# Kernel tuning notes

Hardware: AMD Instinct MI355X
Metric: run time of the kernel (lower is better)

The kernel has to match this reference:

```python
import jax, jax.numpy as jnp
import numpy as np


def _up2(x):
    return jnp.repeat(jnp.repeat(x, 2, axis=2), 2, axis=3)


def setup_inputs() -> dict:
    key = jax.random.key(0)
    ks = jax.random.split(key, 6)
    Vps, C, H, W = 32, 128, 64, 64
    return {
        "x1": jax.random.normal(ks[0], (Vps, C, H, W), dtype=jnp.float32),
        "x2": jax.random.normal(ks[1], (Vps, C, H // 2, W // 2), dtype=jnp.float32),
        "x3": jax.random.normal(ks[2], (Vps, C, H // 4, W // 4), dtype=jnp.float32),
        "x4": jax.random.normal(ks[3], (Vps, C, H // 4, W // 4), dtype=jnp.float32),
        "conv_w": jax.random.normal(ks[4], (128, 512), dtype=jnp.float32) * 0.02,
        "conv_b": jnp.zeros((128,), dtype=jnp.float32),
        "gamma": jnp.zeros((1,), dtype=jnp.float32),
        "weight": jnp.ones((128,), dtype=jnp.float32),
        "lin_w": jax.random.normal(ks[5], (1, 128), dtype=jnp.float32) * 0.1,
    }


def reference(x1, x2, x3, x4, conv_w, conv_b, gamma, weight, lin_w):
    # upsample lower pyramid levels to x1 resolution and concat on channels
    x_sm = jnp.concatenate([x1, _up2(x2), _up2(_up2(x3)), _up2(_up2(x4))], axis=1)
    # 1x1 conv: [Vps,512,H,W] x [128,512] -> [Vps,128,H,W]
    x_sm = jnp.einsum('vchw,oc->vohw', x_sm, conv_w) + conv_b[None, :, None, None]
    Vps, C, H, W = x_sm.shape

    # --- batch (viewport) attention ---
    gap = jnp.mean(x_sm, axis=(2, 3))                     # [Vps, C]
    v_q = gap @ lin_w.T                                    # [Vps, 1]
    att = v_q @ v_q.T                                      # [Vps, Vps]
    att_new = jnp.broadcast_to(jnp.max(att, axis=-1, keepdims=True), att.shape)
    vps_mat = jax.nn.softmax(att_new, axis=-1)             # rows constant -> uniform
    v_v = x_sm.reshape(Vps, C * H * W)
    vps_att = (vps_mat @ v_v).reshape(Vps, C, H, W)
    x_sm = vps_att * gamma + x_sm

    # --- channel attention ---
    c_q = jnp.mean(x_sm, axis=(2, 3))                      # [Vps, C]
    att_C = c_q.T @ c_q                                    # [C, C]
    C_mat = jax.nn.softmax(att_C, axis=-1) * weight        # broadcast over last dim
    c_v = x_sm.reshape(C, Vps * H * W)                     # faithful raw reshape as in torch
    C_att = (C_mat @ c_v).reshape(Vps, C, H, W)
    out = C_att + x_sm
    return out.reshape(Vps, C, H * W)
```

## Files before the change

### kernel.cpp

```cpp
#include <hip/hip_runtime.h>

#define V 32
#define CH 128
#define SP 4096

typedef __attribute__((ext_vector_type(8))) short bf16x8;
typedef __attribute__((ext_vector_type(4))) float f32x4;

__device__ __forceinline__ unsigned short bf16rne(float x) {
    union { float f; unsigned u; } v; v.f = x;
    unsigned r = v.u + 0x7fff + ((v.u >> 16) & 1);
    return (unsigned short)(r >> 16);
}

__device__ __forceinline__ int xswz(int s) { return (s & 7) ^ ((s >> 2) & 7); }

__device__ __forceinline__ const float* xsm_row(const float* xsm, int j, int r) {
    return xsm + ((size_t)((j >> 2) * CH + (j & 3) * 32 + r)) * SP;
}

__global__ __launch_bounds__(256) void prep_w(const float* __restrict__ W,
                                              unsigned short* __restrict__ Wpad)
{
    int row = blockIdx.x;
    int j = threadIdx.x;
    if (j < 136) {
        int sigma = row >> 7, o = row & 127;
        float v = (j < 128) ? W[o * 512 + sigma * 128 + j] : 0.f;
        Wpad[row * 136 + j] = bf16rne(v);
    }
}

__global__ __launch_bounds__(256, 4) void conv_lo(
    const float* __restrict__ xa, const float* __restrict__ xb,
    const unsigned short* __restrict__ WA, const unsigned short* __restrict__ WB,
    int spatial, int nph, float* __restrict__ outbuf)
{
    __shared__ __align__(16) unsigned short Xl[64 * 128];
    const int v = blockIdx.y, sc = blockIdx.x, tid = threadIdx.x;
    const int lane = tid & 63, w = tid >> 6;
    const int l15 = lane & 15, quad = lane >> 4;
    const int o0 = (w >> 1) * 64, s0 = (w & 1) * 32;
    const int sq = tid & 15, cp0 = tid >> 4;

    f32x4 acc[4][2];
#pragma unroll
    for (int it = 0; it < 4; ++it)
#pragma unroll
        for (int st = 0; st < 2; ++st) acc[it][st] = (f32x4){0.f, 0.f, 0.f, 0.f};

#pragma unroll 1
    for (int ph = 0; ph < nph; ++ph) {
        if (ph) __syncthreads();
        const float* xp = ph ? xb : xa;
        const unsigned short* wp = ph ? WB : WA;
        const float* xbase = xp + (size_t)v * CH * spatial + sc * 64;
#pragma unroll
        for (int rep = 0; rep < 4; ++rep) {
            int c = (cp0 + rep * 16) * 2;
            const float* r0 = xbase + (size_t)c * spatial + sq * 4;
            float4 va = *(const float4*)r0;
            float4 vb = *(const float4*)(r0 + spatial);
            float a4[4] = {va.x, va.y, va.z, va.w};
            float b4[4] = {vb.x, vb.y, vb.z, vb.w};
#pragma unroll
            for (int i = 0; i < 4; ++i) {
                int s = sq * 4 + i;
                ushort2 pk; pk.x = bf16rne(a4[i]); pk.y = bf16rne(b4[i]);
                *(ushort2*)&Xl[s * 128 + (((c >> 3) ^ xswz(s)) * 8) + (c & 7)] = pk;
            }
        }
        __syncthreads();
#pragma unroll
        for (int ks = 0; ks < 4; ++ks) {
            int kb = ks * 4 + quad;
            bf16x8 af[4], bfr[2];
#pragma unroll
            for (int it = 0; it < 4; ++it)
                af[it] = *(const bf16x8*)&wp[(o0 + it * 16 + l15) * 136 + ks * 32 + quad * 8];
#pragma unroll
            for (int st = 0; st < 2; ++st) {
                int s = s0 + st * 16 + l15;
                bfr[st] = *(const bf16x8*)&Xl[s * 128 + ((kb ^ xswz(s)) * 8)];
            }
#pragma unroll
            for (int it = 0; it < 4; ++it)
#pragma unroll
                for (int st = 0; st < 2; ++st)
                    acc[it][st] = __builtin_amdgcn_mfma_f32_16x16x32_bf16(
                        bfr[st], af[it], acc[it][st], 0, 0, 0);
        }
    }
#pragma unroll
    for (int it = 0; it < 4; ++it) {
        int o = o0 + it * 16 + l15;
        float* orow = outbuf + ((size_t)(v * CH + o)) * spatial + sc * 64;
#pragma unroll
        for (int st = 0; st < 2; ++st) {
            int sb = s0 + st * 16 + quad * 4;
            *(f32x4*)(orow + sb) = acc[it][st];
        }
    }
}

__global__ __launch_bounds__(256, 4) void conv_full(
    const float* __restrict__ x1, const unsigned short* __restrict__ W0,
    const float* __restrict__ bias, const float* __restrict__ conv2,
    const float* __restrict__ conv34, float* __restrict__ xsm,
    float* __restrict__ gap)
{
    __shared__ __align__(16) unsigned short Xl[64 * 128];
    __shared__ float gscr[4][64];
    const int v = blockIdx.y, sc = blockIdx.x, tid = threadIdx.x;
    const int lane = tid & 63, w = tid >> 6;
    const int l15 = lane & 15, quad = lane >> 4;
    const int o0 = (w >> 1) * 64, s0 = (w & 1) * 32;
    const int sq = tid & 15, cp0 = tid >> 4;

    f32x4 acc[4][2];
#pragma unroll
    for (int it = 0; it < 4; ++it)
#pragma unroll
        for (int st = 0; st < 2; ++st) acc[it][st] = (f32x4){0.f, 0.f, 0.f, 0.f};

    const float* xbase = x1 + (size_t)v * CH * SP + sc * 64;
#pragma unroll
    for (int rep = 0; rep < 4; ++rep) {
        int c = (cp0 + rep * 16) * 2;
        const float* r0 = xbase + (size_t)c * SP + sq * 4;
        float4 va = *(const float4*)r0;
        float4 vb = *(const float4*)(r0 + SP);
        float a4[4] = {va.x, va.y, va.z, va.w};
        float b4[4] = {vb.x, vb.y, vb.z, vb.w};
#pragma unroll
        for (int i = 0; i < 4; ++i) {
            int s = sq * 4 + i;
            ushort2 pk; pk.x = bf16rne(a4[i]); pk.y = bf16rne(b4[i]);
            *(ushort2*)&Xl[s * 128 + (((c >> 3) ^ xswz(s)) * 8) + (c & 7)] = pk;
        }
    }
    __syncthreads();
#pragma unroll
    for (int ks = 0; ks < 4; ++ks) {
        int kb = ks * 4 + quad;
        bf16x8 af[4], bfr[2];
#pragma unroll
        for (int it = 0; it < 4; ++it)
            af[it] = *(const bf16x8*)&W0[(o0 + it * 16 + l15) * 136 + ks * 32 + quad * 8];
#pragma unroll
        for (int st = 0; st < 2; ++st) {
            int s = s0 + st * 16 + l15;
            bfr[st] = *(const bf16x8*)&Xl[s * 128 + ((kb ^ xswz(s)) * 8)];
        }
#pragma unroll
        for (int it = 0; it < 4; ++it)
#pragma unroll
            for (int st = 0; st < 2; ++st)
                acc[it][st] = __builtin_amdgcn_mfma_f32_16x16x32_bf16(
                    bfr[st], af[it], acc[it][st], 0, 0, 0);
    }

    const float* c2row = conv2 + (size_t)v * CH * 1024 + (sc >> 1) * 32;
    const float* c34row = conv34 + (size_t)v * CH * 256 + (sc >> 2) * 16;
    float gs[4];
#pragma unroll
    for (int it = 0; it < 4; ++it) {
        int o = o0 + it * 16 + l15;
        float b = bias[o];
        float* orow = xsm + ((size_t)(v * CH + o)) * SP + sc * 64;
        const float* c2p = c2row + (size_t)o * 1024;
        const float* c34p = c34row + (size_t)o * 256;
        float lsum = 0.f;
#pragma unroll
        for (int st = 0; st < 2; ++st) {
            int sb = s0 + st * 16 + quad * 4;
            float2 c2v = *(const float2*)(c2p + (sb >> 1));
            float c34v = c34p[sb >> 2];
            f32x4 a = acc[it][st];
            f32x4 ov;
            ov[0] = a[0] + b + c2v.x + c34v;
            ov[1] = a[1] + b + c2v.x + c34v;
            ov[2] = a[2] + b + c2v.y + c34v;
            ov[3] = a[3] + b + c2v.y + c34v;
            *(f32x4*)(orow + sb) = ov;
            lsum += ov[0] + ov[1] + ov[2] + ov[3];
        }
        gs[it] = lsum;
    }
#pragma unroll
    for (int m = 16; m < 64; m <<= 1)
#pragma unroll
        for (int k = 0; k < 4; ++k) gs[k] += __shfl_xor(gs[k], m, 64);
    if (quad == 0) {
#pragma unroll
        for (int it = 0; it < 4; ++it)
            gscr[w][it * 16 + l15] = gs[it];
    }
    __syncthreads();
    if (tid < 128) {
        int o = tid, b2 = (o >> 6) * 2;
        atomicAdd(&gap[v * CH + o], gscr[b2][o & 63] + gscr[b2 + 1][o & 63]);
    }
}

__global__ __launch_bounds__(128) void build_G(
    const float* __restrict__ gap, const float* __restrict__ gammap,
    const float* __restrict__ weight, unsigned short* __restrict__ GsPad)
{
    __shared__ float cq[32][128];
    __shared__ float red[128];
    const int i = blockIdx.x, j = threadIdx.x;
    const float g = gammap[0];

    float gb = 0.f;
    for (int v = 0; v < 32; ++v) gb += gap[v * CH + j];
    gb = gb * (1.f / 32.f) * (1.f / 4096.f) * g;
    for (int v = 0; v < 32; ++v) cq[v][j] = gap[v * CH + j] * (1.f / 4096.f) + gb;
    __syncthreads();

    float a = 0.f;
    for (int v = 0; v < 32; ++v) a += cq[v][i] * cq[v][j];

    red[j] = a; __syncthreads();
    float m = -1e30f;
    for (int t = 0; t < 128; ++t) m = fmaxf(m, red[t]);
    __syncthreads();
    float e = __expf(a - m);
    red[j] = e; __syncthreads();
    float ssum = 0.f;
    for (int t = 0; t < 128; ++t) ssum += red[t];
    float cm = e / ssum * weight[j] + ((i == j) ? 1.f : 0.f);
    __syncthreads();
    red[j] = cm; __syncthreads();
    float rs = 0.f;
    for (int t = (j & 3); t < 128; t += 4) rs += red[t];
    float gfull = cm + g * (1.f / 32.f) * rs;
    GsPad[i * 136 + j] = bf16rne(gfull - ((i == j) ? 1.f : 0.f));
}

__global__ __launch_bounds__(256, 4) void apply_G(
    float* __restrict__ xsm, const unsigned short* __restrict__ GsPad)
{
    __shared__ __align__(16) unsigned short Xl[64 * 128];
    const int r = blockIdx.y, sc = blockIdx.x, tid = threadIdx.x;
    const int lane = tid & 63, w = tid >> 6;
    const int l15 = lane & 15, quad = lane >> 4;
    const int i0 = (w >> 1) * 64, s0 = (w & 1) * 32;
    const int sq = tid & 15, cp0 = tid >> 4;

    f32x4 acc[4][2];
#pragma unroll
    for (int it = 0; it < 4; ++it)
#pragma unroll
        for (int st = 0; st < 2; ++st) acc[it][st] = (f32x4){0.f, 0.f, 0.f, 0.f};

#pragma unroll
    for (int rep = 0; rep < 4; ++rep) {
        int c = (cp0 + rep * 16) * 2;
        const float* r0 = xsm_row(xsm, c, r) + sc * 64 + sq * 4;
        const float* r1 = xsm_row(xsm, c + 1, r) + sc * 64 + sq * 4;
        float4 va = *(const float4*)r0;
        float4 vb = *(const float4*)r1;
        float a4[4] = {va.x, va.y, va.z, va.w};
        float b4[4] = {vb.x, vb.y, vb.z, vb.w};
#pragma unroll
        for (int i = 0; i < 4; ++i) {
            int s = sq * 4 + i;
            ushort2 pk; pk.x = bf16rne(a4[i]); pk.y = bf16rne(b4[i]);
            *(ushort2*)&Xl[s * 128 + (((c >> 3) ^ xswz(s)) * 8) + (c & 7)] = pk;
        }
    }
    __syncthreads();
#pragma unroll
    for (int ks = 0; ks < 4; ++ks) {
        int kb = ks * 4 + quad;
        bf16x8 af[4], bfr[2];
#pragma unroll
        for (int it = 0; it < 4; ++it)
            af[it] = *(const bf16x8*)&GsPad[(i0 + it * 16 + l15) * 136 + ks * 32 + quad * 8];
#pragma unroll
        for (int st = 0; st < 2; ++st) {
            int s = s0 + st * 16 + l15;
            bfr[st] = *(const bf16x8*)&Xl[s * 128 + ((kb ^ xswz(s)) * 8)];
        }
#pragma unroll
        for (int it = 0; it < 4; ++it)
#pragma unroll
            for (int st = 0; st < 2; ++st)
                acc[it][st] = __builtin_amdgcn_mfma_f32_16x16x32_bf16(
                    bfr[st], af[it], acc[it][st], 0, 0, 0);
    }
#pragma unroll
    for (int it = 0; it < 4; ++it) {
        int i = i0 + it * 16 + l15;
        float* rowp = (float*)xsm_row(xsm, i, r) + sc * 64;
#pragma unroll
        for (int st = 0; st < 2; ++st) {
            int sb = s0 + st * 16 + quad * 4;
            f32x4 res = *(const f32x4*)(rowp + sb);
            res += acc[it][st];
            *(f32x4*)(rowp + sb) = res;
        }
    }
}

extern "C" void kernel_launch(void* const* d_in, const int* in_sizes, int n_in,
                              void* d_out, int out_size, void* d_ws, size_t ws_size,
                              hipStream_t stream)
{
    const float* x1     = (const float*)d_in[0];
    const float* x2     = (const float*)d_in[1];
    const float* x3     = (const float*)d_in[2];
    const float* x4     = (const float*)d_in[3];
    const float* conv_w = (const float*)d_in[4];
    const float* conv_b = (const float*)d_in[5];
    const float* gamma  = (const float*)d_in[6];
    const float* weight = (const float*)d_in[7];

    float* out = (float*)d_out;
    float* ws  = (float*)d_ws;

    float* conv2  = ws;
    float* conv34 = ws + (size_t)4194304;
    float* gap    = ws + (size_t)5242880;
    unsigned short* Wpad  = (unsigned short*)(ws + (size_t)5246976);
    unsigned short* GsPad = (unsigned short*)(ws + (size_t)5281792);

    hipMemsetAsync(gap, 0, 4096 * sizeof(float), stream);

    prep_w<<<512, 256, 0, stream>>>(conv_w, Wpad);
    conv_lo<<<dim3(16, 32), 256, 0, stream>>>(x2, x2, Wpad + 1 * 128 * 136,
                                              Wpad + 1 * 128 * 136, 1024, 1, conv2);
    conv_lo<<<dim3(4, 32), 256, 0, stream>>>(x3, x4, Wpad + 2 * 128 * 136,
                                             Wpad + 3 * 128 * 136, 256, 2, conv34);
    conv_full<<<dim3(64, 32), 256, 0, stream>>>(x1, Wpad, conv_b, conv2, conv34, out, gap);
    build_G<<<128, 128, 0, stream>>>(gap, gamma, weight, GsPad);
    apply_G<<<dim3(64, 32), 256, 0, stream>>>(out, GsPad);
}
```

Baseline: 230.7 us.

## Make conv_full and apply_G persistent over four tiles with double-buffered LDS prefetch

Result: slower. 238.3 us (+3.3%).

```diff
diff --git a/kernel.cpp b/kernel.cpp
--- a/kernel.cpp
+++ b/kernel.cpp
@@ -31,7 +31,7 @@
     }
 }
 
-__global__ __launch_bounds__(256, 4) void conv_lo(
+__global__ __launch_bounds__(256, 3) void conv_lo(
     const float* __restrict__ xa, const float* __restrict__ xb,
     const unsigned short* __restrict__ WA, const unsigned short* __restrict__ WB,
     int spatial, int nph, float* __restrict__ outbuf)
@@ -54,6 +54,12 @@
         if (ph) __syncthreads();
         const float* xp = ph ? xb : xa;
         const unsigned short* wp = ph ? WB : WA;
+        bf16x8 af[4][4];
+#pragma unroll
+        for (int ks = 0; ks < 4; ++ks)
+#pragma unroll
+            for (int it = 0; it < 4; ++it)
+                af[ks][it] = *(const bf16x8*)&wp[(o0 + it * 16 + l15) * 136 + ks * 32 + quad * 8];
         const float* xbase = xp + (size_t)v * CH * spatial + sc * 64;
 #pragma unroll
         for (int rep = 0; rep < 4; ++rep) {
@@ -74,10 +80,7 @@
 #pragma unroll
         for (int ks = 0; ks < 4; ++ks) {
             int kb = ks * 4 + quad;
-            bf16x8 af[4], bfr[2];
-#pragma unroll
-            for (int it = 0; it < 4; ++it)
-                af[it] = *(const bf16x8*)&wp[(o0 + it * 16 + l15) * 136 + ks * 32 + quad * 8];
+            bf16x8 bfr[2];
 #pragma unroll
             for (int st = 0; st < 2; ++st) {
                 int s = s0 + st * 16 + l15;
@@ -88,7 +91,7 @@
 #pragma unroll
                 for (int st = 0; st < 2; ++st)
                     acc[it][st] = __builtin_amdgcn_mfma_f32_16x16x32_bf16(
-                        bfr[st], af[it], acc[it][st], 0, 0, 0);
+                        bfr[st], af[ks][it], acc[it][st], 0, 0, 0);
         }
     }
 #pragma unroll
@@ -103,103 +106,146 @@
     }
 }
 
-__global__ __launch_bounds__(256, 4) void conv_full(
+__global__ __launch_bounds__(256, 2) void conv_full(
     const float* __restrict__ x1, const unsigned short* __restrict__ W0,
     const float* __restrict__ bias, const float* __restrict__ conv2,
     const float* __restrict__ conv34, float* __restrict__ xsm,
     float* __restrict__ gap)
 {
-    __shared__ __align__(16) unsigned short Xl[64 * 128];
-    __shared__ float gscr[4][64];
-    const int v = blockIdx.y, sc = blockIdx.x, tid = threadIdx.x;
+    __shared__ __align__(16) unsigned short Xl[2][64 * 128];
+    const int vg = blockIdx.y, sc = blockIdx.x, tid = threadIdx.x;
     const int lane = tid & 63, w = tid >> 6;
     const int l15 = lane & 15, quad = lane >> 4;
     const int o0 = (w >> 1) * 64, s0 = (w & 1) * 32;
     const int sq = tid & 15, cp0 = tid >> 4;
 
-    f32x4 acc[4][2];
-#pragma unroll
-    for (int it = 0; it < 4; ++it)
-#pragma unroll
-        for (int st = 0; st < 2; ++st) acc[it][st] = (f32x4){0.f, 0.f, 0.f, 0.f};
-
-    const float* xbase = x1 + (size_t)v * CH * SP + sc * 64;
+    bf16x8 af[4][4];
+#pragma unroll
+    for (int ks = 0; ks < 4; ++ks)
+#pragma unroll
+        for (int it = 0; it < 4; ++it)
+            af[ks][it] = *(const bf16x8*)&W0[(o0 + it * 16 + l15) * 136 + ks * 32 + quad * 8];
+    float bv[4];
+#pragma unroll
+    for (int it = 0; it < 4; ++it) bv[it] = bias[o0 + it * 16 + l15];
+
+    float4 xva[4], xvb[4];
+    {
+        const float* xbase = x1 + (size_t)(vg * 4) * CH * SP + sc * 64;
+#pragma unroll
+        for (int rep = 0; rep < 4; ++rep) {
+            int c = (cp0 + rep * 16) * 2;
+            const float* r0 = xbase + (size_t)c * SP + sq * 4;
+            xva[rep] = *(const float4*)r0;
+            xvb[rep] = *(const float4*)(r0 + SP);
+        }
+    }
 #pragma unroll
     for (int rep = 0; rep < 4; ++rep) {
         int c = (cp0 + rep * 16) * 2;
-        const float* r0 = xbase + (size_t)c * SP + sq * 4;
-        float4 va = *(const float4*)r0;
-        float4 vb = *(const float4*)(r0 + SP);
-        float a4[4] = {va.x, va.y, va.z, va.w};
-        float b4[4] = {vb.x, vb.y, vb.z, vb.w};
+        float a4[4] = {xva[rep].x, xva[rep].y, xva[rep].z, xva[rep].w};
+        float b4[4] = {xvb[rep].x, xvb[rep].y, xvb[rep].z, xvb[rep].w};
 #pragma unroll
         for (int i = 0; i < 4; ++i) {
             int s = sq * 4 + i;
             ushort2 pk; pk.x = bf16rne(a4[i]); pk.y = bf16rne(b4[i]);
-            *(ushort2*)&Xl[s * 128 + (((c >> 3) ^ xswz(s)) * 8) + (c & 7)] = pk;
-        }
-    }
-    __syncthreads();
-#pragma unroll
-    for (int ks = 0; ks < 4; ++ks) {
-        int kb = ks * 4 + quad;
-        bf16x8 af[4], bfr[2];
+            *(ushort2*)&Xl[0][s * 128 + (((c >> 3) ^ xswz(s)) * 8) + (c & 7)] = pk;
+        }
+    }
+
+#pragma unroll 1
+    for (int t = 0; t < 4; ++t) {
+        const int v = vg * 4 + t;
+        __syncthreads();
+        if (t < 3) {
+            const float* xbase = x1 + (size_t)(v + 1) * CH * SP + sc * 64;
+#pragma unroll
+            for (int rep = 0; rep < 4; ++rep) {
+                int c = (cp0 + rep * 16) * 2;
+                const float* r0 = xbase + (size_t)c * SP + sq * 4;
+                xva[rep] = *(const float4*)r0;
+                xvb[rep] = *(const float4*)(r0 + SP);
+            }
+        }
+        const float* c2row = conv2 + (size_t)v * CH * 1024 + (sc >> 1) * 32;
+        const float* c34row = conv34 + (size_t)v * CH * 256 + (sc >> 2) * 16;
+        float2 c2v[4][2]; float c34v[4][2];
+#pragma unroll
+        for (int it = 0; it < 4; ++it) {
+            int o = o0 + it * 16 + l15;
+#pragma unroll
+            for (int st = 0; st < 2; ++st) {
+                int sb = s0 + st * 16 + quad * 4;
+                c2v[it][st] = *(const float2*)(c2row + (size_t)o * 1024 + (sb >> 1));
+                c34v[it][st] = c34row[(size_t)o * 256 + (sb >> 2)];
+            }
+        }
+        f32x4 acc[4][2];
 #pragma unroll
         for (int it = 0; it < 4; ++it)
-            af[it] = *(const bf16x8*)&W0[(o0 + it * 16 + l15) * 136 + ks * 32 + quad * 8];
-#pragma unroll
-        for (int st = 0; st < 2; ++st) {
-            int s = s0 + st * 16 + l15;
-            bfr[st] = *(const bf16x8*)&Xl[s * 128 + ((kb ^ xswz(s)) * 8)];
-        }
-#pragma unroll
-        for (int it = 0; it < 4; ++it)
-#pragma unroll
-            for (int st = 0; st < 2; ++st)
-                acc[it][st] = __builtin_amdgcn_mfma_f32_16x16x32_bf16(
-                    bfr[st], af[it], acc[it][st], 0, 0, 0);
-    }
-
-    const float* c2row = conv2 + (size_t)v * CH * 1024 + (sc >> 1) * 32;
-    const float* c34row = conv34 + (size_t)v * CH * 256 + (sc >> 2) * 16;
-    float gs[4];
-#pragma unroll
-    for (int it = 0; it < 4; ++it) {
-        int o = o0 + it * 16 + l15;
-        float b = bias[o];
-        float* orow = xsm + ((size_t)(v * CH + o)) * SP + sc * 64;
-        const float* c2p = c2row + (size_t)o * 1024;
-        const float* c34p = c34row + (size_t)o * 256;
-        float lsum = 0.f;
-#pragma unroll
-        for (int st = 0; st < 2; ++st) {
-            int sb = s0 + st * 16 + quad * 4;
-            float2 c2v = *(const float2*)(c2p + (sb >> 1));
-            float c34v = c34p[sb >> 2];
-            f32x4 a = acc[it][st];
-            f32x4 ov;
-            ov[0] = a[0] + b + c2v.x + c34v;
-            ov[1] = a[1] + b + c2v.x + c34v;
-            ov[2] = a[2] + b + c2v.y + c34v;
-            ov[3] = a[3] + b + c2v.y + c34v;
-            *(f32x4*)(orow + sb) = ov;
-            lsum += ov[0] + ov[1] + ov[2] + ov[3];
-        }
-        gs[it] = lsum;
-    }
-#pragma unroll
-    for (int m = 16; m < 64; m <<= 1)
-#pragma unroll
-        for (int k = 0; k < 4; ++k) gs[k] += __shfl_xor(gs[k], m, 64);
-    if (quad == 0) {
-#pragma unroll
-        for (int it = 0; it < 4; ++it)
-            gscr[w][it * 16 + l15] = gs[it];
-    }
-    __syncthreads();
-    if (tid < 128) {
-        int o = tid, b2 = (o >> 6) * 2;
-        atomicAdd(&gap[v * CH + o], gscr[b2][o & 63] + gscr[b2 + 1][o & 63]);
+#pragma unroll
+            for (int st = 0; st < 2; ++st) acc[it][st] = (f32x4){0.f, 0.f, 0.f, 0.f};
+        const unsigned short* Xcur = &Xl[t & 1][0];
+#pragma unroll
+        for (int ks = 0; ks < 4; ++ks) {
+            int kb = ks * 4 + quad;
+            bf16x8 bfr[2];
+#pragma unroll
+            for (int st = 0; st < 2; ++st) {
+                int s = s0 + st * 16 + l15;
+                bfr[st] = *(const bf16x8*)&Xcur[s * 128 + ((kb ^ xswz(s)) * 8)];
+            }
+#pragma unroll
+            for (int it = 0; it < 4; ++it)
+#pragma unroll
+                for (int st = 0; st < 2; ++st)
+                    acc[it][st] = __builtin_amdgcn_mfma_f32_16x16x32_bf16(
+                        bfr[st], af[ks][it], acc[it][st], 0, 0, 0);
+        }
+        float gs[4];
+#pragma unroll
+        for (int it = 0; it < 4; ++it) {
+            int o = o0 + it * 16 + l15;
+            float b = bv[it];
+            float* orow = xsm + ((size_t)(v * CH + o)) * SP + sc * 64;
+            float lsum = 0.f;
+#pragma unroll
+            for (int st = 0; st < 2; ++st) {
+                int sb = s0 + st * 16 + quad * 4;
+                f32x4 a = acc[it][st];
+                f32x4 ov;
+                ov[0] = a[0] + b + c2v[it][st].x + c34v[it][st];
+                ov[1] = a[1] + b + c2v[it][st].x + c34v[it][st];
+                ov[2] = a[2] + b + c2v[it][st].y + c34v[it][st];
+                ov[3] = a[3] + b + c2v[it][st].y + c34v[it][st];
+                *(f32x4*)(orow + sb) = ov;
+                lsum += ov[0] + ov[1] + ov[2] + ov[3];
+            }
+            gs[it] = lsum;
+        }
+#pragma unroll
+        for (int m = 16; m < 64; m <<= 1)
+#pragma unroll
+            for (int k = 0; k < 4; ++k) gs[k] += __shfl_xor(gs[k], m, 64);
+        if (quad == 0) {
+#pragma unroll
+            for (int it = 0; it < 4; ++it)
+                atomicAdd(&gap[v * CH + o0 + it * 16 + l15], gs[it]);
+        }
+        if (t < 3) {
+#pragma unroll
+            for (int rep = 0; rep < 4; ++rep) {
+                int c = (cp0 + rep * 16) * 2;
+                float a4[4] = {xva[rep].x, xva[rep].y, xva[rep].z, xva[rep].w};
+                float b4[4] = {xvb[rep].x, xvb[rep].y, xvb[rep].z, xvb[rep].w};
+#pragma unroll
+                for (int i = 0; i < 4; ++i) {
+                    int s = sq * 4 + i;
+                    ushort2 pk; pk.x = bf16rne(a4[i]); pk.y = bf16rne(b4[i]);
+                    *(ushort2*)&Xl[(t + 1) & 1][s * 128 + (((c >> 3) ^ xswz(s)) * 8) + (c & 7)] = pk;
+                }
+            }
+        }
     }
 }
 
@@ -238,68 +284,115 @@
     GsPad[i * 136 + j] = bf16rne(gfull - ((i == j) ? 1.f : 0.f));
 }
 
-__global__ __launch_bounds__(256, 4) void apply_G(
+__global__ __launch_bounds__(256, 2) void apply_G(
     float* __restrict__ xsm, const unsigned short* __restrict__ GsPad)
 {
-    __shared__ __align__(16) unsigned short Xl[64 * 128];
-    const int r = blockIdx.y, sc = blockIdx.x, tid = threadIdx.x;
+    __shared__ __align__(16) unsigned short Xl[2][64 * 128];
+    const int r = blockIdx.y, scg = blockIdx.x, tid = threadIdx.x;
     const int lane = tid & 63, w = tid >> 6;
     const int l15 = lane & 15, quad = lane >> 4;
     const int i0 = (w >> 1) * 64, s0 = (w & 1) * 32;
     const int sq = tid & 15, cp0 = tid >> 4;
 
-    f32x4 acc[4][2];
-#pragma unroll
-    for (int it = 0; it < 4; ++it)
-#pragma unroll
-        for (int st = 0; st < 2; ++st) acc[it][st] = (f32x4){0.f, 0.f, 0.f, 0.f};
-
+    bf16x8 af[4][4];
+#pragma unroll
+    for (int ks = 0; ks < 4; ++ks)
+#pragma unroll
+        for (int it = 0; it < 4; ++it)
+            af[ks][it] = *(const bf16x8*)&GsPad[(i0 + it * 16 + l15) * 136 + ks * 32 + quad * 8];
+
+    float4 xva[4], xvb[4];
+    {
+        const int sc = scg * 4;
+#pragma unroll
+        for (int rep = 0; rep < 4; ++rep) {
+            int c = (cp0 + rep * 16) * 2;
+            xva[rep] = *(const float4*)(xsm_row(xsm, c, r) + sc * 64 + sq * 4);
+            xvb[rep] = *(const float4*)(xsm_row(xsm, c + 1, r) + sc * 64 + sq * 4);
+        }
+    }
 #pragma unroll
     for (int rep = 0; rep < 4; ++rep) {
         int c = (cp0 + rep * 16) * 2;
-        const float* r0 = xsm_row(xsm, c, r) + sc * 64 + sq * 4;
-        const float* r1 = xsm_row(xsm, c + 1, r) + sc * 64 + sq * 4;
-        float4 va = *(const float4*)r0;
-        float4 vb = *(const float4*)r1;
-        float a4[4] = {va.x, va.y, va.z, va.w};
-        float b4[4] = {vb.x, vb.y, vb.z, vb.w};
+        float a4[4] = {xva[rep].x, xva[rep].y, xva[rep].z, xva[rep].w};
+        float b4[4] = {xvb[rep].x, xvb[rep].y, xvb[rep].z, xvb[rep].w};
 #pragma unroll
         for (int i = 0; i < 4; ++i) {
             int s = sq * 4 + i;
             ushort2 pk; pk.x = bf16rne(a4[i]); pk.y = bf16rne(b4[i]);
-            *(ushort2*)&Xl[s * 128 + (((c >> 3) ^ xswz(s)) * 8) + (c & 7)] = pk;
-        }
-    }
-    __syncthreads();
-#pragma unroll
-    for (int ks = 0; ks < 4; ++ks) {
-        int kb = ks * 4 + quad;
-        bf16x8 af[4], bfr[2];
+            *(ushort2*)&Xl[0][s * 128 + (((c >> 3) ^ xswz(s)) * 8) + (c & 7)] = pk;
+        }
+    }
+
+#pragma unroll 1
+    for (int t = 0; t < 4; ++t) {
+        const int sc = scg * 4 + t;
+        __syncthreads();
+        if (t < 3) {
+#pragma unroll
+            for (int rep = 0; rep < 4; ++rep) {
+                int c = (cp0 + rep * 16) * 2;
+                xva[rep] = *(const float4*)(xsm_row(xsm, c, r) + (sc + 1) * 64 + sq * 4);
+                xvb[rep] = *(const float4*)(xsm_row(xsm, c + 1, r) + (sc + 1) * 64 + sq * 4);
+            }
+        }
+        f32x4 resv[4][2];
+#pragma unroll
+        for (int it = 0; it < 4; ++it) {
+            int i = i0 + it * 16 + l15;
+            const float* rowp = xsm_row(xsm, i, r) + sc * 64;
+#pragma unroll
+            for (int st = 0; st < 2; ++st) {
+                int sb = s0 + st * 16 + quad * 4;
+                resv[it][st] = *(const f32x4*)(rowp + sb);
+            }
+        }
+        f32x4 acc[4][2];
 #pragma unroll
         for (int it = 0; it < 4; ++it)
-            af[it] = *(const bf16x8*)&GsPad[(i0 + it * 16 + l15) * 136 + ks * 32 + quad * 8];
-#pragma unroll
-        for (int st = 0; st < 2; ++st) {
-            int s = s0 + st * 16 + l15;
-            bfr[st] = *(const bf16x8*)&Xl[s * 128 + ((kb ^ xswz(s)) * 8)];
-        }
-#pragma unroll
-        for (int it = 0; it < 4; ++it)
-#pragma unroll
-            for (int st = 0; st < 2; ++st)
-                acc[it][st] = __builtin_amdgcn_mfma_f32_16x16x32_bf16(
-                    bfr[st], af[it], acc[it][st], 0, 0, 0);
-    }
-#pragma unroll
-    for (int it = 0; it < 4; ++it) {
-        int i = i0 + it * 16 + l15;
-        float* rowp = (float*)xsm_row(xsm, i, r) + sc * 64;
-#pragma unroll
-        for (int st = 0; st < 2; ++st) {
-            int sb = s0 + st * 16 + quad * 4;
-            f32x4 res = *(const f32x4*)(rowp + sb);
-            res += acc[it][st];
-            *(f32x4*)(rowp + sb) = res;
+#pragma unroll
+            for (int st = 0; st < 2; ++st) acc[it][st] = (f32x4){0.f, 0.f, 0.f, 0.f};
+        const unsigned short* Xcur = &Xl[t & 1][0];
+#pragma unroll
+        for (int ks = 0; ks < 4; ++ks) {
+            int kb = ks * 4 + quad;
+            bf16x8 bfr[2];
+#pragma unroll
+            for (int st = 0; st < 2; ++st) {
+                int s = s0 + st * 16 + l15;
+                bfr[st] = *(const bf16x8*)&Xcur[s * 128 + ((kb ^ xswz(s)) * 8)];
+            }
+#pragma unroll
+            for (int it = 0; it < 4; ++it)
+#pragma unroll
+                for (int st = 0; st < 2; ++st)
+                    acc[it][st] = __builtin_amdgcn_mfma_f32_16x16x32_bf16(
+                        bfr[st], af[ks][it], acc[it][st], 0, 0, 0);
+        }
+#pragma unroll
+        for (int it = 0; it < 4; ++it) {
+            int i = i0 + it * 16 + l15;
+            float* rowp = (float*)xsm_row(xsm, i, r) + sc * 64;
+#pragma unroll
+            for (int st = 0; st < 2; ++st) {
+                int sb = s0 + st * 16 + quad * 4;
+                f32x4 res = resv[it][st] + acc[it][st];
+                *(f32x4*)(rowp + sb) = res;
+            }
+        }
+        if (t < 3) {
+#pragma unroll
+            for (int rep = 0; rep < 4; ++rep) {
+                int c = (cp0 + rep * 16) * 2;
+                float a4[4] = {xva[rep].x, xva[rep].y, xva[rep].z, xva[rep].w};
+                float b4[4] = {xvb[rep].x, xvb[rep].y, xvb[rep].z, xvb[rep].w};
+#pragma unroll
+                for (int i = 0; i < 4; ++i) {
+                    int s = sq * 4 + i;
+                    ushort2 pk; pk.x = bf16rne(a4[i]); pk.y = bf16rne(b4[i]);
+                    *(ushort2*)&Xl[(t + 1) & 1][s * 128 + (((c >> 3) ^ xswz(s)) * 8) + (c & 7)] = pk;
+                }
+            }
         }
     }
 }
@@ -333,7 +426,7 @@
                                               Wpad + 1 * 128 * 136, 1024, 1, conv2);
     conv_lo<<<dim3(4, 32), 256, 0, stream>>>(x3, x4, Wpad + 2 * 128 * 136,
                                              Wpad + 3 * 128 * 136, 256, 2, conv34);
-    conv_full<<<dim3(64, 32), 256, 0, stream>>>(x1, Wpad, conv_b, conv2, conv34, out, gap);
+    conv_full<<<dim3(64, 8), 256, 0, stream>>>(x1, Wpad, conv_b, conv2, conv34, out, gap);
     build_G<<<128, 128, 0, stream>>>(gap, gamma, weight, GsPad);
-    apply_G<<<dim3(64, 32), 256, 0, stream>>>(out, GsPad);
-}
+    apply_G<<<dim3(16, 32), 256, 0, stream>>>(out, GsPad);
+}
```

## Load conv/apply operands directly from global into MFMA registers, drop LDS staging

Applied to the files above, without the earlier changes.

Result: slower. 244.6 us (+6.0%).

```diff
diff --git a/kernel.cpp b/kernel.cpp
--- a/kernel.cpp
+++ b/kernel.cpp
@@ -12,8 +12,6 @@
     unsigned r = v.u + 0x7fff + ((v.u >> 16) & 1);
     return (unsigned short)(r >> 16);
 }
-
-__device__ __forceinline__ int xswz(int s) { return (s & 7) ^ ((s >> 2) & 7); }
 
 __device__ __forceinline__ const float* xsm_row(const float* xsm, int j, int r) {
     return xsm + ((size_t)((j >> 2) * CH + (j & 3) * 32 + r)) * SP;
@@ -31,17 +29,15 @@
     }
 }
 
-__global__ __launch_bounds__(256, 4) void conv_lo(
+__global__ __launch_bounds__(256, 2) void conv_lo(
     const float* __restrict__ xa, const float* __restrict__ xb,
     const unsigned short* __restrict__ WA, const unsigned short* __restrict__ WB,
     int spatial, int nph, float* __restrict__ outbuf)
 {
-    __shared__ __align__(16) unsigned short Xl[64 * 128];
     const int v = blockIdx.y, sc = blockIdx.x, tid = threadIdx.x;
     const int lane = tid & 63, w = tid >> 6;
     const int l15 = lane & 15, quad = lane >> 4;
     const int o0 = (w >> 1) * 64, s0 = (w & 1) * 32;
-    const int sq = tid & 15, cp0 = tid >> 4;
 
     f32x4 acc[4][2];
 #pragma unroll
@@ -51,44 +47,35 @@
 
 #pragma unroll 1
     for (int ph = 0; ph < nph; ++ph) {
-        if (ph) __syncthreads();
         const float* xp = ph ? xb : xa;
         const unsigned short* wp = ph ? WB : WA;
-        const float* xbase = xp + (size_t)v * CH * spatial + sc * 64;
-#pragma unroll
-        for (int rep = 0; rep < 4; ++rep) {
-            int c = (cp0 + rep * 16) * 2;
-            const float* r0 = xbase + (size_t)c * spatial + sq * 4;
-            float4 va = *(const float4*)r0;
-            float4 vb = *(const float4*)(r0 + spatial);
-            float a4[4] = {va.x, va.y, va.z, va.w};
-            float b4[4] = {vb.x, vb.y, vb.z, vb.w};
-#pragma unroll
-            for (int i = 0; i < 4; ++i) {
-                int s = sq * 4 + i;
-                ushort2 pk; pk.x = bf16rne(a4[i]); pk.y = bf16rne(b4[i]);
-                *(ushort2*)&Xl[s * 128 + (((c >> 3) ^ xswz(s)) * 8) + (c & 7)] = pk;
+        bf16x8 af[4][4];
+#pragma unroll
+        for (int ks = 0; ks < 4; ++ks)
+#pragma unroll
+            for (int it = 0; it < 4; ++it)
+                af[ks][it] = *(const bf16x8*)&wp[(o0 + it * 16 + l15) * 136 + ks * 32 + quad * 8];
+        const float* xcol = xp + (size_t)v * CH * spatial + sc * 64;
+#pragma unroll
+        for (int st = 0; st < 2; ++st) {
+            const int sA = s0 + st * 16 + l15;
+            const float* xs = xcol + sA + (size_t)(quad * 8) * spatial;
+            float xr[4][8];
+#pragma unroll
+            for (int ks = 0; ks < 4; ++ks)
+#pragma unroll
+                for (int jj = 0; jj < 8; ++jj)
+                    xr[ks][jj] = xs[(size_t)(ks * 32 + jj) * spatial];
+#pragma unroll
+            for (int ks = 0; ks < 4; ++ks) {
+                bf16x8 bx;
+#pragma unroll
+                for (int jj = 0; jj < 8; ++jj) bx[jj] = (short)bf16rne(xr[ks][jj]);
+#pragma unroll
+                for (int it = 0; it < 4; ++it)
+                    acc[it][st] = __builtin_amdgcn_mfma_f32_16x16x32_bf16(
+                        bx, af[ks][it], acc[it][st], 0, 0, 0);
             }
-        }
-        __syncthreads();
-#pragma unroll
-        for (int ks = 0; ks < 4; ++ks) {
-            int kb = ks * 4 + quad;
-            bf16x8 af[4], bfr[2];
-#pragma unroll
-            for (int it = 0; it < 4; ++it)
-                af[it] = *(const bf16x8*)&wp[(o0 + it * 16 + l15) * 136 + ks * 32 + quad * 8];
-#pragma unroll
-            for (int st = 0; st < 2; ++st) {
-                int s = s0 + st * 16 + l15;
-                bfr[st] = *(const bf16x8*)&Xl[s * 128 + ((kb ^ xswz(s)) * 8)];
-            }
-#pragma unroll
-            for (int it = 0; it < 4; ++it)
-#pragma unroll
-                for (int st = 0; st < 2; ++st)
-                    acc[it][st] = __builtin_amdgcn_mfma_f32_16x16x32_bf16(
-                        bfr[st], af[it], acc[it][st], 0, 0, 0);
         }
     }
 #pragma unroll
@@ -103,19 +90,26 @@
     }
 }
 
-__global__ __launch_bounds__(256, 4) void conv_full(
+__global__ __launch_bounds__(256, 2) void conv_full(
     const float* __restrict__ x1, const unsigned short* __restrict__ W0,
     const float* __restrict__ bias, const float* __restrict__ conv2,
     const float* __restrict__ conv34, float* __restrict__ xsm,
     float* __restrict__ gap)
 {
-    __shared__ __align__(16) unsigned short Xl[64 * 128];
-    __shared__ float gscr[4][64];
     const int v = blockIdx.y, sc = blockIdx.x, tid = threadIdx.x;
     const int lane = tid & 63, w = tid >> 6;
     const int l15 = lane & 15, quad = lane >> 4;
     const int o0 = (w >> 1) * 64, s0 = (w & 1) * 32;
-    const int sq = tid & 15, cp0 = tid >> 4;
+
+    bf16x8 af[4][4];
+#pragma unroll
+    for (int ks = 0; ks < 4; ++ks)
+#pragma unroll
+        for (int it = 0; it < 4; ++it)
+            af[ks][it] = *(const bf16x8*)&W0[(o0 + it * 16 + l15) * 136 + ks * 32 + quad * 8];
+    float bv[4];
+#pragma unroll
+    for (int it = 0; it < 4; ++it) bv[it] = bias[o0 + it * 16 + l15];
 
     f32x4 acc[4][2];
 #pragma unroll
@@ -123,41 +117,27 @@
 #pragma unroll
         for (int st = 0; st < 2; ++st) acc[it][st] = (f32x4){0.f, 0.f, 0.f, 0.f};
 
-    const float* xbase = x1 + (size_t)v * CH * SP + sc * 64;
-#pragma unroll
-    for (int rep = 0; rep < 4; ++rep) {
-        int c = (cp0 + rep * 16) * 2;
-        const float* r0 = xbase + (size_t)c * SP + sq * 4;
-        float4 va = *(const float4*)r0;
-        float4 vb = *(const float4*)(r0 + SP);
-        float a4[4] = {va.x, va.y, va.z, va.w};
-        float b4[4] = {vb.x, vb.y, vb.z, vb.w};
-#pragma unroll
-        for (int i = 0; i < 4; ++i) {
-            int s = sq * 4 + i;
-            ushort2 pk; pk.x = bf16rne(a4[i]); pk.y = bf16rne(b4[i]);
-            *(ushort2*)&Xl[s * 128 + (((c >> 3) ^ xswz(s)) * 8) + (c & 7)] = pk;
-        }
-    }
-    __syncthreads();
-#pragma unroll
-    for (int ks = 0; ks < 4; ++ks) {
-        int kb = ks * 4 + quad;
-        bf16x8 af[4], bfr[2];
-#pragma unroll
-        for (int it = 0; it < 4; ++it)
-            af[it] = *(const bf16x8*)&W0[(o0 + it * 16 + l15) * 136 + ks * 32 + quad * 8];
-#pragma unroll
-        for (int st = 0; st < 2; ++st) {
-            int s = s0 + st * 16 + l15;
-            bfr[st] = *(const bf16x8*)&Xl[s * 128 + ((kb ^ xswz(s)) * 8)];
-        }
-#pragma unroll
-        for (int it = 0; it < 4; ++it)
-#pragma unroll
-            for (int st = 0; st < 2; ++st)
+    const float* xcol = x1 + (size_t)v * CH * SP + sc * 64;
+#pragma unroll
+    for (int st = 0; st < 2; ++st) {
+        const int sA = s0 + st * 16 + l15;
+        const float* xs = xcol + sA + (size_t)(quad * 8) * SP;
+        float xr[4][8];
+#pragma unroll
+        for (int ks = 0; ks < 4; ++ks)
+#pragma unroll
+            for (int jj = 0; jj < 8; ++jj)
+                xr[ks][jj] = xs[(size_t)(ks * 32 + jj) * SP];
+#pragma unroll
+        for (int ks = 0; ks < 4; ++ks) {
+            bf16x8 bx;
+#pragma unroll
+            for (int jj = 0; jj < 8; ++jj) bx[jj] = (short)bf16rne(xr[ks][jj]);
+#pragma unroll
+            for (int it = 0; it < 4; ++it)
                 acc[it][st] = __builtin_amdgcn_mfma_f32_16x16x32_bf16(
-                    bfr[st], af[it], acc[it][st], 0, 0, 0);
+                    bx, af[ks][it], acc[it][st], 0, 0, 0);
+        }
     }
 
     const float* c2row = conv2 + (size_t)v * CH * 1024 + (sc >> 1) * 32;
@@ -166,7 +146,7 @@
 #pragma unroll
     for (int it = 0; it < 4; ++it) {
         int o = o0 + it * 16 + l15;
-        float b = bias[o];
+        float b = bv[it];
         float* orow = xsm + ((size_t)(v * CH + o)) * SP + sc * 64;
         const float* c2p = c2row + (size_t)o * 1024;
         const float* c34p = c34row + (size_t)o * 256;
@@ -194,12 +174,7 @@
     if (quad == 0) {
 #pragma unroll
         for (int it = 0; it < 4; ++it)
-            gscr[w][it * 16 + l15] = gs[it];
-    }
-    __syncthreads();
-    if (tid < 128) {
-        int o = tid, b2 = (o >> 6) * 2;
-        atomicAdd(&gap[v * CH + o], gscr[b2][o & 63] + gscr[b2 + 1][o & 63]);
+            atomicAdd(&gap[v * CH + o0 + it * 16 + l15], gs[it]);
     }
 }
 
@@ -238,15 +213,20 @@
     GsPad[i * 136 + j] = bf16rne(gfull - ((i == j) ? 1.f : 0.f));
 }
 
-__global__ __launch_bounds__(256, 4) void apply_G(
+__global__ __launch_bounds__(256, 2) void apply_G(
     float* __restrict__ xsm, const unsigned short* __restrict__ GsPad)
 {
-    __shared__ __align__(16) unsigned short Xl[64 * 128];
     const int r = blockIdx.y, sc = blockIdx.x, tid = threadIdx.x;
     const int lane = tid & 63, w = tid >> 6;
     const int l15 = lane & 15, quad = lane >> 4;
     const int i0 = (w >> 1) * 64, s0 = (w & 1) * 32;
-    const int sq = tid & 15, cp0 = tid >> 4;
+
+    bf16x8 af[4][4];
+#pragma unroll
+    for (int ks = 0; ks < 4; ++ks)
+#pragma unroll
+        for (int it = 0; it < 4; ++it)
+            af[ks][it] = *(const bf16x8*)&GsPad[(i0 + it * 16 + l15) * 136 + ks * 32 + quad * 8];
 
     f32x4 acc[4][2];
 #pragma unroll
@@ -255,41 +235,30 @@
         for (int st = 0; st < 2; ++st) acc[it][st] = (f32x4){0.f, 0.f, 0.f, 0.f};
 
 #pragma unroll
-    for (int rep = 0; rep < 4; ++rep) {
-        int c = (cp0 + rep * 16) * 2;
-        const float* r0 = xsm_row(xsm, c, r) + sc * 64 + sq * 4;
-        const float* r1 = xsm_row(xsm, c + 1, r) + sc * 64 + sq * 4;
-        float4 va = *(const float4*)r0;
-        float4 vb = *(const float4*)r1;
-        float a4[4] = {va.x, va.y, va.z, va.w};
-        float b4[4] = {vb.x, vb.y, vb.z, vb.w};
-#pragma unroll
-        for (int i = 0; i < 4; ++i) {
-            int s = sq * 4 + i;
-            ushort2 pk; pk.x = bf16rne(a4[i]); pk.y = bf16rne(b4[i]);
-            *(ushort2*)&Xl[s * 128 + (((c >> 3) ^ xswz(s)) * 8) + (c & 7)] = pk;
-        }
-    }
+    for (int st = 0; st < 2; ++st) {
+        const int sA = sc * 64 + s0 + st * 16 + l15;
+        float xr[4][8];
+#pragma unroll
+        for (int ks = 0; ks < 4; ++ks)
+#pragma unroll
+            for (int jj = 0; jj < 8; ++jj) {
+                int j = ks * 32 + quad * 8 + jj;
+                xr[ks][jj] = xsm_row(xsm, j, r)[sA];
+            }
+#pragma unroll
+        for (int ks = 0; ks < 4; ++ks) {
+            bf16x8 bx;
+#pragma unroll
+            for (int jj = 0; jj < 8; ++jj) bx[jj] = (short)bf16rne(xr[ks][jj]);
+#pragma unroll
+            for (int it = 0; it < 4; ++it)
+                acc[it][st] = __builtin_amdgcn_mfma_f32_16x16x32_bf16(
+                    bx, af[ks][it], acc[it][st], 0, 0, 0);
+        }
+    }
+
     __syncthreads();
-#pragma unroll
-    for (int ks = 0; ks < 4; ++ks) {
-        int kb = ks * 4 + quad;
-        bf16x8 af[4], bfr[2];
-#pragma unroll
-        for (int it = 0; it < 4; ++it)
-            af[it] = *(const bf16x8*)&GsPad[(i0 + it * 16 + l15) * 136 + ks * 32 + quad * 8];
-#pragma unroll
-        for (int st = 0; st < 2; ++st) {
-            int s = s0 + st * 16 + l15;
-            bfr[st] = *(const bf16x8*)&Xl[s * 128 + ((kb ^ xswz(s)) * 8)];
-        }
-#pragma unroll
-        for (int it = 0; it < 4; ++it)
-#pragma unroll
-            for (int st = 0; st < 2; ++st)
-                acc[it][st] = __builtin_amdgcn_mfma_f32_16x16x32_bf16(
-                    bfr[st], af[it], acc[it][st], 0, 0, 0);
-    }
+
 #pragma unroll
     for (int it = 0; it < 4; ++it) {
         int i = i0 + it * 16 + l15;
```

## Fuse pyramid-level convs into one full-res kernel with LDS-staged weights

Applied to the files above, without the earlier changes.

Result: slower. 242.9 us (+5.3%).

```diff
diff --git a/kernel.cpp b/kernel.cpp
--- a/kernel.cpp
+++ b/kernel.cpp
@@ -31,11 +31,13 @@
     }
 }
 
-__global__ __launch_bounds__(256, 4) void conv_lo(
-    const float* __restrict__ xa, const float* __restrict__ xb,
-    const unsigned short* __restrict__ WA, const unsigned short* __restrict__ WB,
-    int spatial, int nph, float* __restrict__ outbuf)
-{
+__global__ __launch_bounds__(256) void conv_full(
+    const float* __restrict__ x1, const float* __restrict__ x2,
+    const float* __restrict__ x3, const float* __restrict__ x4,
+    const unsigned short* __restrict__ Wpad, const float* __restrict__ bias,
+    float* __restrict__ xsm, float* __restrict__ gap)
+{
+    __shared__ __align__(16) unsigned short Wl[128 * 136];
     __shared__ __align__(16) unsigned short Xl[64 * 128];
     const int v = blockIdx.y, sc = blockIdx.x, tid = threadIdx.x;
     const int lane = tid & 63, w = tid >> 6;
@@ -50,19 +52,37 @@
         for (int st = 0; st < 2; ++st) acc[it][st] = (f32x4){0.f, 0.f, 0.f, 0.f};
 
 #pragma unroll 1
-    for (int ph = 0; ph < nph; ++ph) {
-        if (ph) __syncthreads();
-        const float* xp = ph ? xb : xa;
-        const unsigned short* wp = ph ? WB : WA;
-        const float* xbase = xp + (size_t)v * CH * spatial + sc * 64;
+    for (int sigma = 0; sigma < 4; ++sigma) {
+        if (sigma) __syncthreads();
+        {
+            const float4* wsrc = (const float4*)(Wpad + sigma * 128 * 136);
+            float4* wdst = (float4*)Wl;
+            for (int idx = tid; idx < 2176; idx += 256) wdst[idx] = wsrc[idx];
+        }
 #pragma unroll
         for (int rep = 0; rep < 4; ++rep) {
             int c = (cp0 + rep * 16) * 2;
-            const float* r0 = xbase + (size_t)c * spatial + sq * 4;
-            float4 va = *(const float4*)r0;
-            float4 vb = *(const float4*)(r0 + spatial);
-            float a4[4] = {va.x, va.y, va.z, va.w};
-            float b4[4] = {vb.x, vb.y, vb.z, vb.w};
+            float a4[4], b4[4];
+            if (sigma == 0) {
+                const float* p = x1 + (size_t)(v * CH + c) * SP + sc * 64 + sq * 4;
+                float4 va = *(const float4*)p;
+                float4 vb = *(const float4*)(p + SP);
+                a4[0] = va.x; a4[1] = va.y; a4[2] = va.z; a4[3] = va.w;
+                b4[0] = vb.x; b4[1] = vb.y; b4[2] = vb.z; b4[3] = vb.w;
+            } else if (sigma == 1) {
+                const float* p = x2 + (size_t)(v * CH + c) * 1024 + (sc >> 1) * 32 + sq * 2;
+                float2 fa = *(const float2*)p;
+                float2 fb = *(const float2*)(p + 1024);
+                a4[0] = fa.x; a4[1] = fa.x; a4[2] = fa.y; a4[3] = fa.y;
+                b4[0] = fb.x; b4[1] = fb.x; b4[2] = fb.y; b4[3] = fb.y;
+            } else {
+                const float* xp = (sigma == 2) ? x3 : x4;
+                const float* p = xp + (size_t)(v * CH + c) * 256 + (sc >> 2) * 16 + sq;
+                float fa = *p;
+                float fb = *(p + 256);
+                a4[0] = fa; a4[1] = fa; a4[2] = fa; a4[3] = fa;
+                b4[0] = fb; b4[1] = fb; b4[2] = fb; b4[3] = fb;
+            }
 #pragma unroll
             for (int i = 0; i < 4; ++i) {
                 int s = sq * 4 + i;
@@ -77,7 +97,7 @@
             bf16x8 af[4], bfr[2];
 #pragma unroll
             for (int it = 0; it < 4; ++it)
-                af[it] = *(const bf16x8*)&wp[(o0 + it * 16 + l15) * 136 + ks * 32 + quad * 8];
+                af[it] = *(const bf16x8*)&Wl[(o0 + it * 16 + l15) * 136 + ks * 32 + quad * 8];
 #pragma unroll
             for (int st = 0; st < 2; ++st) {
                 int s = s0 + st * 16 + l15;
@@ -91,97 +111,20 @@
                         bfr[st], af[it], acc[it][st], 0, 0, 0);
         }
     }
-#pragma unroll
-    for (int it = 0; it < 4; ++it) {
-        int o = o0 + it * 16 + l15;
-        float* orow = outbuf + ((size_t)(v * CH + o)) * spatial + sc * 64;
-#pragma unroll
-        for (int st = 0; st < 2; ++st) {
-            int sb = s0 + st * 16 + quad * 4;
-            *(f32x4*)(orow + sb) = acc[it][st];
-        }
-    }
-}
-
-__global__ __launch_bounds__(256, 4) void conv_full(
-    const float* __restrict__ x1, const unsigned short* __restrict__ W0,
-    const float* __restrict__ bias, const float* __restrict__ conv2,
-    const float* __restrict__ conv34, float* __restrict__ xsm,
-    float* __restrict__ gap)
-{
-    __shared__ __align__(16) unsigned short Xl[64 * 128];
-    __shared__ float gscr[4][64];
-    const int v = blockIdx.y, sc = blockIdx.x, tid = threadIdx.x;
-    const int lane = tid & 63, w = tid >> 6;
-    const int l15 = lane & 15, quad = lane >> 4;
-    const int o0 = (w >> 1) * 64, s0 = (w & 1) * 32;
-    const int sq = tid & 15, cp0 = tid >> 4;
-
-    f32x4 acc[4][2];
-#pragma unroll
-    for (int it = 0; it < 4; ++it)
-#pragma unroll
-        for (int st = 0; st < 2; ++st) acc[it][st] = (f32x4){0.f, 0.f, 0.f, 0.f};
-
-    const float* xbase = x1 + (size_t)v * CH * SP + sc * 64;
-#pragma unroll
-    for (int rep = 0; rep < 4; ++rep) {
-        int c = (cp0 + rep * 16) * 2;
-        const float* r0 = xbase + (size_t)c * SP + sq * 4;
-        float4 va = *(const float4*)r0;
-        float4 vb = *(const float4*)(r0 + SP);
-        float a4[4] = {va.x, va.y, va.z, va.w};
-        float b4[4] = {vb.x, vb.y, vb.z, vb.w};
-#pragma unroll
-        for (int i = 0; i < 4; ++i) {
-            int s = sq * 4 + i;
-            ushort2 pk; pk.x = bf16rne(a4[i]); pk.y = bf16rne(b4[i]);
-            *(ushort2*)&Xl[s * 128 + (((c >> 3) ^ xswz(s)) * 8) + (c & 7)] = pk;
-        }
-    }
-    __syncthreads();
-#pragma unroll
-    for (int ks = 0; ks < 4; ++ks) {
-        int kb = ks * 4 + quad;
-        bf16x8 af[4], bfr[2];
-#pragma unroll
-        for (int it = 0; it < 4; ++it)
-            af[it] = *(const bf16x8*)&W0[(o0 + it * 16 + l15) * 136 + ks * 32 + quad * 8];
-#pragma unroll
-        for (int st = 0; st < 2; ++st) {
-            int s = s0 + st * 16 + l15;
-            bfr[st] = *(const bf16x8*)&Xl[s * 128 + ((kb ^ xswz(s)) * 8)];
-        }
-#pragma unroll
-        for (int it = 0; it < 4; ++it)
-#pragma unroll
-            for (int st = 0; st < 2; ++st)
-                acc[it][st] = __builtin_amdgcn_mfma_f32_16x16x32_bf16(
-                    bfr[st], af[it], acc[it][st], 0, 0, 0);
-    }
-
-    const float* c2row = conv2 + (size_t)v * CH * 1024 + (sc >> 1) * 32;
-    const float* c34row = conv34 + (size_t)v * CH * 256 + (sc >> 2) * 16;
+
     float gs[4];
 #pragma unroll
     for (int it = 0; it < 4; ++it) {
         int o = o0 + it * 16 + l15;
         float b = bias[o];
         float* orow = xsm + ((size_t)(v * CH + o)) * SP + sc * 64;
-        const float* c2p = c2row + (size_t)o * 1024;
-        const float* c34p = c34row + (size_t)o * 256;
         float lsum = 0.f;
 #pragma unroll
         for (int st = 0; st < 2; ++st) {
             int sb = s0 + st * 16 + quad * 4;
-            float2 c2v = *(const float2*)(c2p + (sb >> 1));
-            float c34v = c34p[sb >> 2];
             f32x4 a = acc[it][st];
             f32x4 ov;
-            ov[0] = a[0] + b + c2v.x + c34v;
-            ov[1] = a[1] + b + c2v.x + c34v;
-            ov[2] = a[2] + b + c2v.y + c34v;
-            ov[3] = a[3] + b + c2v.y + c34v;
+            ov[0] = a[0] + b; ov[1] = a[1] + b; ov[2] = a[2] + b; ov[3] = a[3] + b;
             *(f32x4*)(orow + sb) = ov;
             lsum += ov[0] + ov[1] + ov[2] + ov[3];
         }
@@ -194,12 +137,7 @@
     if (quad == 0) {
 #pragma unroll
         for (int it = 0; it < 4; ++it)
-            gscr[w][it * 16 + l15] = gs[it];
-    }
-    __syncthreads();
-    if (tid < 128) {
-        int o = tid, b2 = (o >> 6) * 2;
-        atomicAdd(&gap[v * CH + o], gscr[b2][o & 63] + gscr[b2 + 1][o & 63]);
+            atomicAdd(&gap[v * CH + o0 + it * 16 + l15], gs[it]);
     }
 }
 
@@ -238,9 +176,10 @@
     GsPad[i * 136 + j] = bf16rne(gfull - ((i == j) ? 1.f : 0.f));
 }
 
-__global__ __launch_bounds__(256, 4) void apply_G(
+__global__ __launch_bounds__(256) void apply_G(
     float* __restrict__ xsm, const unsigned short* __restrict__ GsPad)
 {
+    __shared__ __align__(16) unsigned short Gl[128 * 136];
     __shared__ __align__(16) unsigned short Xl[64 * 128];
     const int r = blockIdx.y, sc = blockIdx.x, tid = threadIdx.x;
     const int lane = tid & 63, w = tid >> 6;
@@ -254,6 +193,11 @@
 #pragma unroll
         for (int st = 0; st < 2; ++st) acc[it][st] = (f32x4){0.f, 0.f, 0.f, 0.f};
 
+    {
+        const float4* gsrc = (const float4*)GsPad;
+        float4* gdst = (float4*)Gl;
+        for (int idx = tid; idx < 2176; idx += 256) gdst[idx] = gsrc[idx];
+    }
 #pragma unroll
     for (int rep = 0; rep < 4; ++rep) {
         int c = (cp0 + rep * 16) * 2;
@@ -277,7 +221,7 @@
         bf16x8 af[4], bfr[2];
 #pragma unroll
         for (int it = 0; it < 4; ++it)
-            af[it] = *(const bf16x8*)&GsPad[(i0 + it * 16 + l15) * 136 + ks * 32 + quad * 8];
+            af[it] = *(const bf16x8*)&Gl[(i0 + it * 16 + l15) * 136 + ks * 32 + quad * 8];
 #pragma unroll
         for (int st = 0; st < 2; ++st) {
             int s = s0 + st * 16 + l15;
@@ -320,20 +264,14 @@
     float* out = (float*)d_out;
     float* ws  = (float*)d_ws;
 
-    float* conv2  = ws;
-    float* conv34 = ws + (size_t)4194304;
-    float* gap    = ws + (size_t)5242880;
-    unsigned short* Wpad  = (unsigned short*)(ws + (size_t)5246976);
-    unsigned short* GsPad = (unsigned short*)(ws + (size_t)5281792);
+    float* gap = ws;
+    unsigned short* Wpad  = (unsigned short*)(ws + (size_t)4096);
+    unsigned short* GsPad = (unsigned short*)(ws + (size_t)38912);
 
     hipMemsetAsync(gap, 0, 4096 * sizeof(float), stream);
 
     prep_w<<<512, 256, 0, stream>>>(conv_w, Wpad);
-    conv_lo<<<dim3(16, 32), 256, 0, stream>>>(x2, x2, Wpad + 1 * 128 * 136,
-                                              Wpad + 1 * 128 * 136, 1024, 1, conv2);
-    conv_lo<<<dim3(4, 32), 256, 0, stream>>>(x3, x4, Wpad + 2 * 128 * 136,
-                                             Wpad + 3 * 128 * 136, 256, 2, conv34);
-    conv_full<<<dim3(64, 32), 256, 0, stream>>>(x1, Wpad, conv_b, conv2, conv34, out, gap);
+    conv_full<<<dim3(64, 32), 256, 0, stream>>>(x1, x2, x3, x4, Wpad, conv_b, out, gap);
     build_G<<<128, 128, 0, stream>>>(gap, gamma, weight, GsPad);
     apply_G<<<dim3(64, 32), 256, 0, stream>>>(out, GsPad);
 }
```
